# Kernel tuning notes

Measured on AMD Instinct MI355X. Metric: run time of the kernel, lower is better.

Reference implementation:

```python
import jax, jax.numpy as jnp
import numpy as np

NUM_HEADS = 16

def setup_inputs() -> dict:
    key = jax.random.key(0)
    k1, k2, k3, k4 = jax.random.split(key, 4)
    B, N, D = 4, 2048, 1024
    x = jax.random.normal(k1, (B, N, D), dtype=jnp.float32)
    s = 1.0 / np.sqrt(D)
    W_qkv = jax.random.normal(k2, (D, 3 * D), dtype=jnp.float32) * s
    W_proj = jax.random.normal(k3, (D, D), dtype=jnp.float32) * s
    b_proj = jax.random.normal(k4, (D,), dtype=jnp.float32) * 0.01
    return {"x": x, "W_qkv": W_qkv, "W_proj": W_proj, "b_proj": b_proj}

def reference(x, W_qkv, W_proj, b_proj):
    B, N, D = x.shape
    H = NUM_HEADS
    hd = D // H
    scale = hd ** (-0.5)
    qkv = x @ W_qkv  # [B, N, 3D]
    qkv = qkv.reshape(B, N, 3, H, hd).transpose(2, 0, 3, 1, 4)  # [3, B, H, N, hd]
    q, k, v = qkv[0], qkv[1], qkv[2]
    attn = jnp.einsum('bhqd,bhkd->bhqk', q, k) * scale  # [B, H, N, N]
    attn = jax.nn.softmax(attn, axis=-1)
    out = jnp.einsum('bhqk,bhkd->bhqd', attn, v)  # [B, H, N, hd]
    out = out.transpose(0, 2, 1, 3).reshape(B, N, D)
    return out @ W_proj + b_proj
```

## Files before the change

kernel.cpp:

```cpp
#include <hip/hip_runtime.h>
#include <hip/hip_bf16.h>

constexpr int B  = 4;
constexpr int N  = 2048;
constexpr int D  = 1024;
constexpr int H  = 16;
constexpr int HD = 64;
constexpr int M  = B * N;
constexpr int K3 = 3 * D;

typedef __attribute__((ext_vector_type(8))) short  short8v;
typedef __attribute__((ext_vector_type(4))) float  f32x4;
typedef __attribute__((ext_vector_type(4))) unsigned short us4;

__device__ inline unsigned short f2bf(float f) {
    union { float f; unsigned u; } x{f};
    unsigned r = x.u + 0x7fffu + ((x.u >> 16) & 1u);
    return (unsigned short)(r >> 16);
}

__device__ __forceinline__ void gload_lds16(const unsigned short* g, unsigned short* l) {
    __builtin_amdgcn_global_load_lds(
        (const __attribute__((address_space(1))) void*)g,
        (__attribute__((address_space(3))) void*)l, 16, 0, 0);
}

__global__ __launch_bounds__(256)
void cvt_bf16(const float* __restrict__ in, unsigned short* __restrict__ outp, int n8) {
    int i = blockIdx.x * 256 + threadIdx.x;
    if (i >= n8) return;
    f32x4 a = *(const f32x4*)(in + (size_t)i * 8);
    f32x4 b = *(const f32x4*)(in + (size_t)i * 8 + 4);
    short8v v;
    #pragma unroll
    for (int j = 0; j < 4; ++j) { v[j] = (short)f2bf(a[j]); v[4 + j] = (short)f2bf(b[j]); }
    *(short8v*)(outp + (size_t)i * 8) = v;
}

__global__ __launch_bounds__(256)
void transpose_w(const float* __restrict__ W, unsigned short* __restrict__ Wt,
                 int Kd, int Nd) {
    __shared__ unsigned short t[64][68];
    const int k0 = blockIdx.y * 64, n0 = blockIdx.x * 64;
    const int tid = threadIdx.x;
    #pragma unroll
    for (int i = 0; i < 4; ++i) {
        int k = (tid >> 4) + 16 * i, nn = (tid & 15) * 4;
        f32x4 v = *(const f32x4*)(W + (size_t)(k0 + k) * Nd + n0 + nn);
        #pragma unroll
        for (int j = 0; j < 4; ++j) t[k][nn + j] = f2bf(v[j]);
    }
    __syncthreads();
    #pragma unroll
    for (int i = 0; i < 4; ++i) {
        int n = (tid >> 4) + 16 * i, kk = (tid & 15) * 4;
        us4 v = { t[kk][n], t[kk + 1][n], t[kk + 2][n], t[kk + 3][n] };
        *(us4*)(Wt + (size_t)(n0 + n) * Kd + k0 + kk) = v;
    }
}

template <bool BIAS, typename OutT>
__global__ __launch_bounds__(256)
void gemm_bf16(const unsigned short* __restrict__ A,
               const unsigned short* __restrict__ Bt,
               OutT* __restrict__ C, const float* __restrict__ bias,
               int Md, int Nd, int Kd) {
    __shared__ unsigned short As[128 * 64];
    __shared__ unsigned short Bs[128 * 64];

    const int tid  = threadIdx.x;
    const int lane = tid & 63;
    const int w    = tid >> 6;
    const int lr   = lane & 15;
    const int lg   = lane >> 4;
    const int wm   = w >> 1, wn = w & 1;
    const int row0 = blockIdx.y * 128;
    const int col0 = blockIdx.x * 128;

    f32x4 acc[4][4] = {};

    for (int k0 = 0; k0 < Kd; k0 += 64) {
        #pragma unroll
        for (int it = 0; it < 4; ++it) {
            const int c    = (it * 4 + w) * 64 + lane;
            const int row  = c >> 3, slot = c & 7;
            const int gs   = (slot ^ (row & 7)) * 8;
            gload_lds16(A  + (size_t)(row0 + row) * Kd + k0 + gs, As + c * 8);
            gload_lds16(Bt + (size_t)(col0 + row) * Kd + k0 + gs, Bs + c * 8);
        }
        asm volatile("s_waitcnt vmcnt(0)" ::: "memory");
        __syncthreads();

        short8v af[4][2], bfr[4][2];
        #pragma unroll
        for (int mi = 0; mi < 4; ++mi) {
            const int row = wm * 64 + mi * 16 + lr;
            #pragma unroll
            for (int kk = 0; kk < 2; ++kk)
                af[mi][kk] = *(const short8v*)(As + row * 64 + (((kk * 4 + lg) ^ (row & 7)) * 8));
        }
        #pragma unroll
        for (int ni = 0; ni < 4; ++ni) {
            const int col = wn * 64 + ni * 16 + lr;
            #pragma unroll
            for (int kk = 0; kk < 2; ++kk)
                bfr[ni][kk] = *(const short8v*)(Bs + col * 64 + (((kk * 4 + lg) ^ (col & 7)) * 8));
        }

        #pragma unroll
        for (int kk = 0; kk < 2; ++kk)
            #pragma unroll
            for (int mi = 0; mi < 4; ++mi)
                #pragma unroll
                for (int ni = 0; ni < 4; ++ni)
                    acc[mi][ni] = __builtin_amdgcn_mfma_f32_16x16x32_bf16(
                        af[mi][kk], bfr[ni][kk], acc[mi][ni], 0, 0, 0);

        __syncthreads();
    }

    #pragma unroll
    for (int mi = 0; mi < 4; ++mi) {
        #pragma unroll
        for (int r = 0; r < 4; ++r) {
            const size_t row = row0 + wm * 64 + mi * 16 + 4 * lg + r;
            #pragma unroll
            for (int ni = 0; ni < 4; ++ni) {
                const int col = col0 + wn * 64 + ni * 16 + lr;
                float v = acc[mi][ni][r];
                if constexpr (BIAS) v += bias[col];
                if constexpr (sizeof(OutT) == 2)
                    C[row * (size_t)Nd + col] = (OutT)f2bf(v);
                else
                    C[row * (size_t)Nd + col] = (OutT)v;
            }
        }
    }
}

__global__ __launch_bounds__(256)
void transposeV(const unsigned short* __restrict__ qkvb, unsigned short* __restrict__ Vt) {
    __shared__ unsigned short t[64][68];
    const int bh = blockIdx.y, b = bh >> 4, h = bh & 15;
    const int n0 = blockIdx.x * 64;
    const int tid = threadIdx.x;

    #pragma unroll
    for (int i = 0; i < 4; ++i) {
        int key = (tid >> 4) + 16 * i, d0 = (tid & 15) * 4;
        us4 v = *(const us4*)(qkvb + (size_t)(b * N + n0 + key) * K3 + 2 * D + h * 64 + d0);
        *(us4*)&t[key][d0] = v;
    }
    __syncthreads();
    #pragma unroll
    for (int i = 0; i < 4; ++i) {
        int d = (tid >> 4) + 16 * i, k0 = (tid & 15) * 4;
        us4 v = { t[k0][d], t[k0 + 1][d], t[k0 + 2][d], t[k0 + 3][d] };
        *(us4*)(Vt + ((size_t)bh * 64 + d) * N + n0 + k0) = v;
    }
}

__global__ __launch_bounds__(256)
void attn_mfma(const unsigned short* __restrict__ qkvb,
               const unsigned short* __restrict__ Vt,
               unsigned short* __restrict__ out) {
    __shared__ unsigned short K_lds[64 * 64];
    __shared__ unsigned short V_lds[64 * 64];
    __shared__ unsigned short P_lds[4 * 16 * 64];

    const int tid  = threadIdx.x;
    const int lane = tid & 63;
    const int w    = tid >> 6;
    const int lr   = lane & 15;
    const int lg   = lane >> 4;
    const int bh   = blockIdx.y, b = bh >> 4, h = bh & 15;
    const int q0   = blockIdx.x * 64;

    short8v qa[2];
    {
        const unsigned short* qrow =
            qkvb + (size_t)(b * N + q0 + w * 16 + lr) * K3 + h * 64 + lg * 8;
        qa[0] = *(const short8v*)(qrow);
        qa[1] = *(const short8v*)(qrow + 32);
    }

    f32x4 oacc[4] = {};
    float mrow = -1e30f;
    float lsum = 0.f;

    const unsigned short* kbase  = qkvb + (size_t)b * N * K3 + D + h * 64;
    const unsigned short* vtbase = Vt + (size_t)bh * 64 * N;

    for (int kt = 0; kt < N; kt += 64) {
        __syncthreads();
        #pragma unroll
        for (int i = 0; i < 2; ++i) {
            const int c   = tid + 256 * i;
            const int row = c >> 3, slot = c & 7;
            const int gs  = (slot ^ (row & 7)) * 8;
            gload_lds16(kbase  + (size_t)(kt + row) * K3 + gs, K_lds + c * 8);
            gload_lds16(vtbase + (size_t)row * N + kt + gs,    V_lds + c * 8);
        }
        asm volatile("s_waitcnt vmcnt(0)" ::: "memory");
        __syncthreads();

        f32x4 sacc[4] = {};
        #pragma unroll
        for (int sj = 0; sj < 4; ++sj) {
            const int key = 16 * sj + lr;
            #pragma unroll
            for (int ks = 0; ks < 2; ++ks) {
                short8v kb = *(const short8v*)(K_lds + key * 64 +
                                               (((4 * ks + lg) ^ (key & 7)) * 8));
                sacc[sj] = __builtin_amdgcn_mfma_f32_16x16x32_bf16(kb, qa[ks], sacc[sj], 0, 0, 0);
            }
        }

        float pmax = fmaxf(fmaxf(sacc[0][0], sacc[0][1]), fmaxf(sacc[0][2], sacc[0][3]));
        #pragma unroll
        for (int sj = 1; sj < 4; ++sj)
            pmax = fmaxf(pmax, fmaxf(fmaxf(sacc[sj][0], sacc[sj][1]),
                                     fmaxf(sacc[sj][2], sacc[sj][3])));
        pmax = fmaxf(pmax, __shfl_xor(pmax, 16));
        pmax = fmaxf(pmax, __shfl_xor(pmax, 32));

        if (!__all(pmax - mrow <= 64.0f)) {
            const float mnew  = fmaxf(mrow, pmax);
            const float alpha = __expf((mrow - mnew) * 0.125f);
            mrow = mnew;
            lsum *= alpha;
            #pragma unroll
            for (int r = 0; r < 4; ++r) {
                const float ar = __shfl(alpha, 4 * lg + r);
                #pragma unroll
                for (int dj = 0; dj < 4; ++dj) oacc[dj][r] *= ar;
            }
        }

        const float m8 = mrow * 0.125f;
        #pragma unroll
        for (int sj = 0; sj < 4; ++sj) {
            const float p0 = __expf(fmaf(sacc[sj][0], 0.125f, -m8));
            const float p1 = __expf(fmaf(sacc[sj][1], 0.125f, -m8));
            const float p2 = __expf(fmaf(sacc[sj][2], 0.125f, -m8));
            const float p3 = __expf(fmaf(sacc[sj][3], 0.125f, -m8));
            lsum += (p0 + p1) + (p2 + p3);
            unsigned pk0, pk1;
            asm("v_cvt_pk_bf16_f32 %0, %1, %2" : "=v"(pk0) : "v"(p0), "v"(p1));
            asm("v_cvt_pk_bf16_f32 %0, %1, %2" : "=v"(pk1) : "v"(p2), "v"(p3));
            const int t = 2 * sj + (lg >> 1);
            uint2* dst = (uint2*)(P_lds + w * 1024 + lr * 64 +
                                  ((t ^ (lr & 7)) * 8) + 4 * (lg & 1));
            *dst = make_uint2(pk0, pk1);
        }

        #pragma unroll
        for (int ks = 0; ks < 2; ++ks) {
            short8v pa = *(const short8v*)(P_lds + w * 1024 + lr * 64 +
                                           (((4 * ks + lg) ^ (lr & 7)) * 8));
            #pragma unroll
            for (int dj = 0; dj < 4; ++dj) {
                const int d = 16 * dj + lr;
                short8v vb = *(const short8v*)(V_lds + d * 64 +
                                               (((4 * ks + lg) ^ (d & 7)) * 8));
                oacc[dj] = __builtin_amdgcn_mfma_f32_16x16x32_bf16(pa, vb, oacc[dj], 0, 0, 0);
            }
        }
    }

    float ltot = lsum;
    ltot += __shfl_xor(ltot, 16);
    ltot += __shfl_xor(ltot, 32);
    const float linv = 1.0f / ltot;
    #pragma unroll
    for (int r = 0; r < 4; ++r) {
        const float inv = __shfl(linv, 4 * lg + r);
        const int q = q0 + w * 16 + 4 * lg + r;
        #pragma unroll
        for (int dj = 0; dj < 4; ++dj)
            out[((size_t)b * N + q) * D + h * 64 + 16 * dj + lr] = f2bf(oacc[dj][r] * inv);
    }
}

extern "C" void kernel_launch(void* const* d_in, const int* in_sizes, int n_in,
                              void* d_out, int out_size, void* d_ws, size_t ws_size,
                              hipStream_t stream) {
    const float* x     = (const float*)d_in[0];
    const float* Wqkv  = (const float*)d_in[1];
    const float* Wproj = (const float*)d_in[2];
    const float* bproj = (const float*)d_in[3];
    float* outp = (float*)d_out;

    unsigned short* x_bf    = (unsigned short*)d_ws;
    unsigned short* Wqkv_t  = x_bf + (size_t)M * D;
    unsigned short* Wproj_t = Wqkv_t + (size_t)K3 * D;
    unsigned short* qkv_bf  = Wproj_t + (size_t)D * D;
    unsigned short* Vtp     = qkv_bf + (size_t)M * K3;
    unsigned short* ao_bf   = Vtp + (size_t)B * H * HD * N;

    cvt_bf16<<<(M * D / 8 + 255) / 256, 256, 0, stream>>>(x, x_bf, M * D / 8);
    transpose_w<<<dim3(K3 / 64, D / 64), 256, 0, stream>>>(Wqkv, Wqkv_t, D, K3);
    transpose_w<<<dim3(D / 64, D / 64), 256, 0, stream>>>(Wproj, Wproj_t, D, D);

    dim3 g1(K3 / 128, M / 128);
    gemm_bf16<false, unsigned short><<<g1, 256, 0, stream>>>(x_bf, Wqkv_t, qkv_bf, nullptr, M, K3, D);

    dim3 g2(N / 64, B * H);
    transposeV<<<g2, 256, 0, stream>>>(qkv_bf, Vtp);

    dim3 g3(N / 64, B * H);
    attn_mfma<<<g3, 256, 0, stream>>>(qkv_bf, Vtp, ao_bf);

    dim3 g4(D / 128, M / 128);
    gemm_bf16<true, float><<<g4, 256, 0, stream>>>(ao_bf, Wproj_t, outp, bproj, M, D, D);
}
```

Measured before the change: 317.2 us.

## Double-buffer K/V tiles in attention with prefetch, exp2 softmax, and setprio around MFMAs

Gives the attention kernel two K and V LDS buffers and issues the global-to-LDS loads for the next key tile before computing on the current one, so memory latency can overlap the MFMA and softmax work. Each iteration now ends with one wait and barrier instead of a barrier before and after the load. The exponentials use exp2f with log2(e) folded into the scale, the row max uses a max3-friendly chain, and s_setprio raises wave priority around the MFMA blocks. The second buffer doubles K/V LDS use, which may reduce occupancy.

Result: slower. 343.1 us (+8.2%).

```diff
diff --git a/kernel.cpp b/kernel.cpp
--- a/kernel.cpp
+++ b/kernel.cpp
@@ -23,6 +23,10 @@
     __builtin_amdgcn_global_load_lds(
         (const __attribute__((address_space(1))) void*)g,
         (__attribute__((address_space(3))) void*)l, 16, 0, 0);
+}
+
+__device__ __forceinline__ float max3f(float a, float b, float c) {
+    return fmaxf(fmaxf(a, b), c);
 }
 
 __global__ __launch_bounds__(256)
@@ -164,8 +168,8 @@
 void attn_mfma(const unsigned short* __restrict__ qkvb,
                const unsigned short* __restrict__ Vt,
                unsigned short* __restrict__ out) {
-    __shared__ unsigned short K_lds[64 * 64];
-    __shared__ unsigned short V_lds[64 * 64];
+    __shared__ unsigned short K_lds[2][64 * 64];
+    __shared__ unsigned short V_lds[2][64 * 64];
     __shared__ unsigned short P_lds[4 * 16 * 64];
 
     const int tid  = threadIdx.x;
@@ -187,46 +191,67 @@
     f32x4 oacc[4] = {};
     float mrow = -1e30f;
     float lsum = 0.f;
+    constexpr float CE = 0.125f * 1.44269504089f;
 
     const unsigned short* kbase  = qkvb + (size_t)b * N * K3 + D + h * 64;
     const unsigned short* vtbase = Vt + (size_t)bh * 64 * N;
 
-    for (int kt = 0; kt < N; kt += 64) {
-        __syncthreads();
-        #pragma unroll
-        for (int i = 0; i < 2; ++i) {
-            const int c   = tid + 256 * i;
-            const int row = c >> 3, slot = c & 7;
-            const int gs  = (slot ^ (row & 7)) * 8;
-            gload_lds16(kbase  + (size_t)(kt + row) * K3 + gs, K_lds + c * 8);
-            gload_lds16(vtbase + (size_t)row * N + kt + gs,    V_lds + c * 8);
-        }
-        asm volatile("s_waitcnt vmcnt(0)" ::: "memory");
-        __syncthreads();
+    const int crow = tid >> 3, cslot = tid & 7;
+    const int gs0  = (cslot ^ (crow & 7)) * 8;
+    const int crow1 = (tid + 256) >> 3;
+    const int gs1  = (cslot ^ (crow1 & 7)) * 8;
+
+    {
+        gload_lds16(kbase  + (size_t)crow  * K3 + gs0, &K_lds[0][tid * 8]);
+        gload_lds16(vtbase + (size_t)crow  * N  + gs0, &V_lds[0][tid * 8]);
+        gload_lds16(kbase  + (size_t)crow1 * K3 + gs1, &K_lds[0][(tid + 256) * 8]);
+        gload_lds16(vtbase + (size_t)crow1 * N  + gs1, &V_lds[0][(tid + 256) * 8]);
+    }
+    asm volatile("s_waitcnt vmcnt(0)\n\ts_barrier" ::: "memory");
+
+    int cur = 0;
+    for (int t = 0; t < N / 64; ++t) {
+        if (t < N / 64 - 1) {
+            const int kt1 = (t + 1) * 64;
+            unsigned short* kd = (unsigned short*)&K_lds[cur ^ 1][0];
+            unsigned short* vd = (unsigned short*)&V_lds[cur ^ 1][0];
+            gload_lds16(kbase  + (size_t)(kt1 + crow)  * K3 + gs0, kd + tid * 8);
+            gload_lds16(vtbase + (size_t)crow  * N + kt1 + gs0,    vd + tid * 8);
+            gload_lds16(kbase  + (size_t)(kt1 + crow1) * K3 + gs1, kd + (tid + 256) * 8);
+            gload_lds16(vtbase + (size_t)crow1 * N + kt1 + gs1,    vd + (tid + 256) * 8);
+        }
+
+        const unsigned short* Kc = &K_lds[cur][0];
+        const unsigned short* Vc = &V_lds[cur][0];
 
         f32x4 sacc[4] = {};
+        __builtin_amdgcn_s_setprio(1);
         #pragma unroll
         for (int sj = 0; sj < 4; ++sj) {
             const int key = 16 * sj + lr;
             #pragma unroll
             for (int ks = 0; ks < 2; ++ks) {
-                short8v kb = *(const short8v*)(K_lds + key * 64 +
+                short8v kb = *(const short8v*)(Kc + key * 64 +
                                                (((4 * ks + lg) ^ (key & 7)) * 8));
                 sacc[sj] = __builtin_amdgcn_mfma_f32_16x16x32_bf16(kb, qa[ks], sacc[sj], 0, 0, 0);
             }
         }
-
-        float pmax = fmaxf(fmaxf(sacc[0][0], sacc[0][1]), fmaxf(sacc[0][2], sacc[0][3]));
-        #pragma unroll
-        for (int sj = 1; sj < 4; ++sj)
-            pmax = fmaxf(pmax, fmaxf(fmaxf(sacc[sj][0], sacc[sj][1]),
-                                     fmaxf(sacc[sj][2], sacc[sj][3])));
+        __builtin_amdgcn_s_setprio(0);
+
+        float pmax = max3f(sacc[0][0], sacc[0][1], sacc[0][2]);
+        pmax = max3f(pmax, sacc[0][3], sacc[1][0]);
+        pmax = max3f(pmax, sacc[1][1], sacc[1][2]);
+        pmax = max3f(pmax, sacc[1][3], sacc[2][0]);
+        pmax = max3f(pmax, sacc[2][1], sacc[2][2]);
+        pmax = max3f(pmax, sacc[2][3], sacc[3][0]);
+        pmax = max3f(pmax, sacc[3][1], sacc[3][2]);
+        pmax = fmaxf(pmax, sacc[3][3]);
         pmax = fmaxf(pmax, __shfl_xor(pmax, 16));
         pmax = fmaxf(pmax, __shfl_xor(pmax, 32));
 
         if (!__all(pmax - mrow <= 64.0f)) {
             const float mnew  = fmaxf(mrow, pmax);
-            const float alpha = __expf((mrow - mnew) * 0.125f);
+            const float alpha = exp2f((mrow - mnew) * CE);
             mrow = mnew;
             lsum *= alpha;
             #pragma unroll
@@ -237,23 +262,24 @@
             }
         }
 
-        const float m8 = mrow * 0.125f;
+        const float mc = mrow * CE;
         #pragma unroll
         for (int sj = 0; sj < 4; ++sj) {
-            const float p0 = __expf(fmaf(sacc[sj][0], 0.125f, -m8));
-            const float p1 = __expf(fmaf(sacc[sj][1], 0.125f, -m8));
-            const float p2 = __expf(fmaf(sacc[sj][2], 0.125f, -m8));
-            const float p3 = __expf(fmaf(sacc[sj][3], 0.125f, -m8));
+            const float p0 = exp2f(fmaf(sacc[sj][0], CE, -mc));
+            const float p1 = exp2f(fmaf(sacc[sj][1], CE, -mc));
+            const float p2 = exp2f(fmaf(sacc[sj][2], CE, -mc));
+            const float p3 = exp2f(fmaf(sacc[sj][3], CE, -mc));
             lsum += (p0 + p1) + (p2 + p3);
             unsigned pk0, pk1;
             asm("v_cvt_pk_bf16_f32 %0, %1, %2" : "=v"(pk0) : "v"(p0), "v"(p1));
             asm("v_cvt_pk_bf16_f32 %0, %1, %2" : "=v"(pk1) : "v"(p2), "v"(p3));
-            const int t = 2 * sj + (lg >> 1);
+            const int ts = 2 * sj + (lg >> 1);
             uint2* dst = (uint2*)(P_lds + w * 1024 + lr * 64 +
-                                  ((t ^ (lr & 7)) * 8) + 4 * (lg & 1));
+                                  ((ts ^ (lr & 7)) * 8) + 4 * (lg & 1));
             *dst = make_uint2(pk0, pk1);
         }
 
+        __builtin_amdgcn_s_setprio(1);
         #pragma unroll
         for (int ks = 0; ks < 2; ++ks) {
             short8v pa = *(const short8v*)(P_lds + w * 1024 + lr * 64 +
@@ -261,11 +287,15 @@
             #pragma unroll
             for (int dj = 0; dj < 4; ++dj) {
                 const int d = 16 * dj + lr;
-                short8v vb = *(const short8v*)(V_lds + d * 64 +
+                short8v vb = *(const short8v*)(Vc + d * 64 +
                                                (((4 * ks + lg) ^ (d & 7)) * 8));
                 oacc[dj] = __builtin_amdgcn_mfma_f32_16x16x32_bf16(pa, vb, oacc[dj], 0, 0, 0);
             }
         }
+        __builtin_amdgcn_s_setprio(0);
+
+        asm volatile("s_waitcnt vmcnt(0)\n\ts_barrier" ::: "memory");
+        cur ^= 1;
     }
 
     float ltot = lsum;
```
